# Performance work log

Hardware: AMD Instinct MI355X
Metric: run time of the kernel (lower is better)

## Reference

```python
import jax, jax.numpy as jnp
import numpy as np

NEG_BIG = -9e15
ALPHA = 0.2  # LeakyReLU negative slope


def setup_inputs() -> dict:
    key = jax.random.key(0)
    k1, k2, k3, k4 = jax.random.split(key, 4)
    N, F_in, F_out = 8192, 256, 64
    inp = jax.random.normal(k1, (N, F_in), dtype=jnp.float32)
    adj = jax.random.randint(k2, (N, N), 0, 2, dtype=jnp.int32)
    W = jax.random.normal(k3, (F_in, F_out), dtype=jnp.float32) * 0.05
    a = jax.random.normal(k4, (2 * F_out, 1), dtype=jnp.float32) * 0.05
    return {"input": inp, "adj": adj, "W": W, "a": a}


def reference(input, adj, W, a):
    # h = X W : [N, F_out]
    h = input @ W
    F_out = W.shape[1]
    # a_input[i,j] = concat(h_i, h_j); a_input @ a = h@a1 broadcast over j + h@a2 broadcast over i.
    a1 = a[:F_out, 0]   # [F_out]
    a2 = a[F_out:, 0]   # [F_out]
    s1 = h @ a1         # [N]
    s2 = h @ a2         # [N]
    e = jax.nn.leaky_relu(s1[:, None] + s2[None, :], negative_slope=ALPHA)  # [N, N]
    att = jnp.where(adj > 0, e, jnp.float32(NEG_BIG))
    att = jax.nn.softmax(att, axis=1)
    # dropout is identity in eval mode (training=False)
    h_prime = att @ h   # [N, F_out]
    return jax.nn.elu(h_prime)
```

## Files before the change

kernel.cpp:

```cpp
#include <hip/hip_runtime.h>
#include <hip/hip_bf16.h>

typedef __bf16 bf16_t;
typedef __attribute__((ext_vector_type(8))) __bf16 bf16x8;
typedef __attribute__((ext_vector_type(4))) __bf16 bf16x4;
typedef __attribute__((ext_vector_type(4))) float floatx4;
typedef __attribute__((ext_vector_type(4))) int intx4;

#define NN 8192
#define FIN 256
#define FOUT 64
#define GAT_ALPHA 0.2f
#define JHALF (NN / 2)

__global__ __launch_bounds__(256) void gat_h_kernel(
    const float* __restrict__ input,
    const float* __restrict__ W,
    const float* __restrict__ a,
    bf16_t* __restrict__ hT,
    float* __restrict__ s1g, float* __restrict__ e1g, float* __restrict__ f1g,
    float* __restrict__ s2g, float* __restrict__ e2g, float* __restrict__ f2g)
{
    alignas(16) __shared__ bf16_t in_lds[32][264];
    alignas(16) __shared__ bf16_t wt_lds[64][264];
    __shared__ float h_lds[32][65];

    const int t  = threadIdx.x;
    const int i0 = blockIdx.x * 32;

    #pragma unroll
    for (int v = 0; v < 8; v++) {
        int u  = v * 256 + t;
        int i  = u >> 6;
        int k4 = (u & 63) * 4;
        floatx4 x = *(const floatx4*)(input + (size_t)(i0 + i) * FIN + k4);
        bf16x4 b;
        #pragma unroll
        for (int e = 0; e < 4; e++) b[e] = (bf16_t)x[e];
        *(bf16x4*)(&in_lds[i][k4]) = b;
    }
    #pragma unroll
    for (int v = 0; v < 16; v++) {
        int u  = v * 256 + t;
        int k  = u >> 4;
        int f4 = (u & 15) * 4;
        floatx4 wv = *(const floatx4*)(W + k * FOUT + f4);
        #pragma unroll
        for (int e = 0; e < 4; e++) wt_lds[f4 + e][k] = (bf16_t)wv[e];
    }
    __syncthreads();

    const int wave = t >> 6;
    const int lane = t & 63;
    const int i16  = (wave & 1) * 16;
    const int f32  = (wave >> 1) * 32;
    const int lm   = lane & 15;
    const int lq   = lane >> 4;

    floatx4 acc0 = {0.f, 0.f, 0.f, 0.f};
    floatx4 acc1 = {0.f, 0.f, 0.f, 0.f};
    #pragma unroll
    for (int ks = 0; ks < 8; ks++) {
        int ko = ks * 32 + lq * 8;
        bf16x8 af = *(const bf16x8*)(&in_lds[i16 + lm][ko]);
        bf16x8 b0 = *(const bf16x8*)(&wt_lds[f32 + lm][ko]);
        bf16x8 b1 = *(const bf16x8*)(&wt_lds[f32 + 16 + lm][ko]);
        acc0 = __builtin_amdgcn_mfma_f32_16x16x32_bf16(af, b0, acc0, 0, 0, 0);
        acc1 = __builtin_amdgcn_mfma_f32_16x16x32_bf16(af, b1, acc1, 0, 0, 0);
    }

    #pragma unroll
    for (int c = 0; c < 2; c++) {
        floatx4 acc = c ? acc1 : acc0;
        int f  = f32 + c * 16 + lm;
        int ib = i0 + i16 + lq * 4;
        bf16x4 hp;
        #pragma unroll
        for (int r = 0; r < 4; r++) hp[r] = (bf16_t)acc[r];
        *(bf16x4*)(hT + (size_t)f * NN + ib) = hp;
    }
    #pragma unroll
    for (int c = 0; c < 2; c++) {
        floatx4 acc = c ? acc1 : acc0;
        #pragma unroll
        for (int r = 0; r < 4; r++)
            h_lds[i16 + lq * 4 + r][f32 + c * 16 + lm] = acc[r];
    }
    __syncthreads();

    if (t < 64) {
        int r   = t & 31;
        int sel = t >> 5;
        const float* av = a + sel * FOUT;
        float s = 0.f;
        #pragma unroll 8
        for (int f = 0; f < FOUT; f++) s += h_lds[r][f] * av[f];
        int gi = i0 + r;
        float E = expf(s);
        float F = expf(GAT_ALPHA * s);
        if (sel == 0) { s1g[gi] = s; e1g[gi] = E; f1g[gi] = F; }
        else          { s2g[gi] = s; e2g[gi] = E; f2g[gi] = F; }
    }
}

#define LOAD_CHUNK(J0)                                                         \
    {                                                                          \
        s2v = *(const floatx4*)(s2g + (J0) + 4 * tj);                          \
        e2v = *(const floatx4*)(e2g + (J0) + 4 * tj);                          \
        f2v = *(const floatx4*)(f2g + (J0) + 4 * tj);                          \
        _Pragma("unroll")                                                      \
        for (int it = 0; it < 8; it++)                                         \
            adjv[it] = *(const intx4*)(adj +                                   \
                (size_t)(i0 + it * 4 + ti) * NN + (J0) + 4 * tj);              \
        _Pragma("unroll")                                                      \
        for (int u = 0; u < 8; u++) {                                          \
            int f  = (u * 256 + t) >> 5;                                       \
            int j8 = ((u * 256 + t) & 31) * 8;                                 \
            hv[u] = *(const bf16x8*)(hT + (size_t)f * NN + (J0) + j8);         \
        }                                                                      \
    }

#define CONSUME_CHUNK()                                                        \
    {                                                                          \
        _Pragma("unroll")                                                      \
        for (int it = 0; it < 8; it++) {                                       \
            int r = it * 4 + ti;                                               \
            float s1r = s1_l[r], E1 = e1_l[r], F1 = f1_l[r];                   \
            bf16x4 wq;                                                         \
            float sum = 0.f;                                                   \
            _Pragma("unroll")                                                  \
            for (int e = 0; e < 4; e++) {                                      \
                bool pos = (s1r + s2v[e]) > 0.f;                               \
                float wv = (adjv[it][e] > 0)                                   \
                               ? (pos ? E1 * e2v[e] : F1 * f2v[e]) : 0.f;      \
                bf16_t wb = (bf16_t)wv;                                        \
                wq[e] = wb;                                                    \
                sum += (float)wb;                                              \
            }                                                                  \
            rowsum[it] += sum;                                                 \
            *(bf16x4*)(&w_lds[r][4 * tj]) = wq;                                \
        }                                                                      \
        _Pragma("unroll")                                                      \
        for (int u = 0; u < 8; u++) {                                          \
            int f  = (u * 256 + t) >> 5;                                       \
            int j8 = ((u * 256 + t) & 31) * 8;                                 \
            *(bf16x8*)(&ht_lds[f][j8]) = hv[u];                                \
        }                                                                      \
    }

#define MFMA_CHUNK()                                                           \
    {                                                                          \
        _Pragma("unroll")                                                      \
        for (int ks = 0; ks < 8; ks++) {                                       \
            int ko = ks * 32 + lq * 8;                                         \
            bf16x8 af = *(const bf16x8*)(&w_lds[i16 + lm][ko]);                \
            bf16x8 b0 = *(const bf16x8*)(&ht_lds[f32 + lm][ko]);               \
            bf16x8 b1 = *(const bf16x8*)(&ht_lds[f32 + 16 + lm][ko]);          \
            acc0 = __builtin_amdgcn_mfma_f32_16x16x32_bf16(af, b0, acc0,0,0,0);\
            acc1 = __builtin_amdgcn_mfma_f32_16x16x32_bf16(af, b1, acc1,0,0,0);\
        }                                                                      \
    }

__global__ __launch_bounds__(256, 2) void gat_att_kernel(
    const int* __restrict__ adj,
    const bf16_t* __restrict__ hT,
    const float* __restrict__ s1g, const float* __restrict__ e1g,
    const float* __restrict__ f1g,
    const float* __restrict__ s2g, const float* __restrict__ e2g,
    const float* __restrict__ f2g,
    float* __restrict__ pacc,
    float* __restrict__ prs)
{
    alignas(16) __shared__ bf16_t w_lds[32][264];
    alignas(16) __shared__ bf16_t ht_lds[64][264];
    __shared__ float part[32][66];
    __shared__ float s1_l[32], e1_l[32], f1_l[32];

    const int t     = threadIdx.x;
    const int i0    = blockIdx.x * 32;
    const int half  = blockIdx.y;
    const int jbase = half * JHALF;
    const int tj    = t & 63;
    const int ti    = t >> 6;

    if (t < 32) {
        s1_l[t] = s1g[i0 + t];
        e1_l[t] = e1g[i0 + t];
        f1_l[t] = f1g[i0 + t];
    }

    const int wave = t >> 6;
    const int lane = t & 63;
    const int i16  = (wave & 1) * 16;
    const int f32  = (wave >> 1) * 32;
    const int lm   = lane & 15;
    const int lq   = lane >> 4;

    floatx4 acc0 = {0.f, 0.f, 0.f, 0.f};
    floatx4 acc1 = {0.f, 0.f, 0.f, 0.f};
    float rowsum[8];
    #pragma unroll
    for (int r = 0; r < 8; r++) rowsum[r] = 0.f;

    intx4   adjv[8];
    bf16x8  hv[8];
    floatx4 s2v, e2v, f2v;

    LOAD_CHUNK(jbase);

    for (int j0 = jbase; j0 < jbase + JHALF; j0 += 256) {
        __syncthreads();
        CONSUME_CHUNK();
        if (j0 + 256 < jbase + JHALF)
            LOAD_CHUNK(j0 + 256);
        __syncthreads();
        MFMA_CHUNK();
    }

    #pragma unroll
    for (int it = 0; it < 8; it++) part[it * 4 + ti][tj] = rowsum[it];
    __syncthreads();
    if (t < 32) {
        float s = 0.f;
        #pragma unroll 8
        for (int k = 0; k < 64; k++) s += part[t][k];
        prs[half * NN + i0 + t] = s;
    }

    float* pa = pacc + (size_t)half * NN * FOUT;
    #pragma unroll
    for (int c = 0; c < 2; c++) {
        floatx4 acc = c ? acc1 : acc0;
        int f = f32 + c * 16 + lm;
        #pragma unroll
        for (int r = 0; r < 4; r++) {
            int i = i16 + lq * 4 + r;
            pa[(size_t)(i0 + i) * FOUT + f] = acc[r];
        }
    }
}

__global__ __launch_bounds__(256) void gat_combine_kernel(
    const float* __restrict__ pacc,
    const float* __restrict__ prs,
    float* __restrict__ out)
{
    int idx = blockIdx.x * 256 + threadIdx.x;
    int i   = idx >> 4;
    floatx4 a0 = *(const floatx4*)(pacc + (size_t)idx * 4);
    floatx4 a1 = *(const floatx4*)(pacc + (size_t)NN * FOUT + (size_t)idx * 4);
    float rs   = prs[i] + prs[NN + i];
    float rinv = (rs > 0.f) ? 1.0f / rs : 0.f;
    floatx4 r;
    #pragma unroll
    for (int e = 0; e < 4; e++) {
        float x = (a0[e] + a1[e]) * rinv;
        r[e] = (x > 0.f) ? x : (expf(x) - 1.0f);
    }
    *(floatx4*)(out + (size_t)idx * 4) = r;
}

extern "C" void kernel_launch(void* const* d_in, const int* in_sizes, int n_in,
                              void* d_out, int out_size, void* d_ws, size_t ws_size,
                              hipStream_t stream) {
    const float* input = (const float*)d_in[0];
    const int*   adj   = (const int*)d_in[1];
    const float* W     = (const float*)d_in[2];
    const float* a     = (const float*)d_in[3];
    float*       out   = (float*)d_out;

    char* ws = (char*)d_ws;
    bf16_t* hT  = (bf16_t*)ws;
    float*  s1g = (float*)(ws + (1 << 20));
    float*  e1g = s1g + NN;
    float*  f1g = e1g + NN;
    float*  s2g = f1g + NN;
    float*  e2g = s2g + NN;
    float*  f2g = e2g + NN;
    float*  pacc = f2g + NN;
    float*  prs  = pacc + 2 * NN * FOUT;

    gat_h_kernel<<<NN / 32, 256, 0, stream>>>(input, W, a, hT,
                                              s1g, e1g, f1g, s2g, e2g, f2g);
    dim3 gridB(NN / 32, 2);
    gat_att_kernel<<<gridB, 256, 0, stream>>>(adj, hT,
                                              s1g, e1g, f1g, s2g, e2g, f2g,
                                              pacc, prs);
    gat_combine_kernel<<<NN * FOUT / 4 / 256, 256, 0, stream>>>(pacc, prs, out);
}
```

Before: 390.4 us.

## Restructure attention kernel to register-direct MFMA operands without LDS staging

The attention kernel now has each wave own 16 rows and feed MFMA straight from registers. Attention weights are computed in the A-fragment layout and hT fragments are loaded directly from global memory, which removes the LDS staging and both per-chunk barriers. Leaky-ReLU selection becomes max(E1*e2, F1*f2), and e2/f2 are packed as bf16 pairs, so s1/s2 are no longer loaded. The j dimension is split 8 ways with higher occupancy to add parallelism. In exchange, hT reads are duplicated across waves, partial-sum traffic grows for the combine kernel, and e2/f2 lose precision to bf16.

```diff
diff --git a/kernel.cpp b/kernel.cpp
--- a/kernel.cpp
+++ b/kernel.cpp
@@ -6,20 +6,23 @@
 typedef __attribute__((ext_vector_type(4))) __bf16 bf16x4;
 typedef __attribute__((ext_vector_type(4))) float floatx4;
 typedef __attribute__((ext_vector_type(4))) int intx4;
+typedef __attribute__((ext_vector_type(4))) unsigned int uintx4;
 
 #define NN 8192
 #define FIN 256
 #define FOUT 64
 #define GAT_ALPHA 0.2f
-#define JHALF (NN / 2)
+#define JSPLIT 8
+#define JSEG (NN / JSPLIT)
+#define NSTEP (JSEG / 32)
 
 __global__ __launch_bounds__(256) void gat_h_kernel(
     const float* __restrict__ input,
     const float* __restrict__ W,
     const float* __restrict__ a,
     bf16_t* __restrict__ hT,
-    float* __restrict__ s1g, float* __restrict__ e1g, float* __restrict__ f1g,
-    float* __restrict__ s2g, float* __restrict__ e2g, float* __restrict__ f2g)
+    float* __restrict__ e1g, float* __restrict__ f1g,
+    unsigned* __restrict__ ef2g)
 {
     alignas(16) __shared__ bf16_t in_lds[32][264];
     alignas(16) __shared__ bf16_t wt_lds[64][264];
@@ -98,145 +101,99 @@
         int gi = i0 + r;
         float E = expf(s);
         float F = expf(GAT_ALPHA * s);
-        if (sel == 0) { s1g[gi] = s; e1g[gi] = E; f1g[gi] = F; }
-        else          { s2g[gi] = s; e2g[gi] = E; f2g[gi] = F; }
-    }
-}
-
-#define LOAD_CHUNK(J0)                                                         \
+        if (sel == 0) {
+            e1g[gi] = E; f1g[gi] = F;
+        } else {
+            unsigned eb = __builtin_bit_cast(unsigned short, (bf16_t)E);
+            unsigned fb = __builtin_bit_cast(unsigned short, (bf16_t)F);
+            ef2g[gi] = (fb << 16) | eb;
+        }
+    }
+}
+
+#define LOADS(B, OFF)                                                          \
     {                                                                          \
-        s2v = *(const floatx4*)(s2g + (J0) + 4 * tj);                          \
-        e2v = *(const floatx4*)(e2g + (J0) + 4 * tj);                          \
-        f2v = *(const floatx4*)(f2g + (J0) + 4 * tj);                          \
+        adjb[B][0] = *(const intx4*)(adjrow + (OFF));                          \
+        adjb[B][1] = *(const intx4*)(adjrow + (OFF) + 4);                      \
+        efb[B][0]  = *(const uintx4*)(efp + (OFF));                            \
+        efb[B][1]  = *(const uintx4*)(efp + (OFF) + 4);                        \
         _Pragma("unroll")                                                      \
-        for (int it = 0; it < 8; it++)                                         \
-            adjv[it] = *(const intx4*)(adj +                                   \
-                (size_t)(i0 + it * 4 + ti) * NN + (J0) + 4 * tj);              \
+        for (int c = 0; c < 4; c++)                                            \
+            htb[B][c] = *(const bf16x8*)(htp + (size_t)c * 16 * NN + (OFF));   \
+    }
+
+#define CONSUME(B)                                                             \
+    {                                                                          \
+        bf16x8 wf;                                                             \
         _Pragma("unroll")                                                      \
-        for (int u = 0; u < 8; u++) {                                          \
-            int f  = (u * 256 + t) >> 5;                                       \
-            int j8 = ((u * 256 + t) & 31) * 8;                                 \
-            hv[u] = *(const bf16x8*)(hT + (size_t)f * NN + (J0) + j8);         \
-        }                                                                      \
-    }
-
-#define CONSUME_CHUNK()                                                        \
-    {                                                                          \
-        _Pragma("unroll")                                                      \
-        for (int it = 0; it < 8; it++) {                                       \
-            int r = it * 4 + ti;                                               \
-            float s1r = s1_l[r], E1 = e1_l[r], F1 = f1_l[r];                   \
-            bf16x4 wq;                                                         \
-            float sum = 0.f;                                                   \
-            _Pragma("unroll")                                                  \
-            for (int e = 0; e < 4; e++) {                                      \
-                bool pos = (s1r + s2v[e]) > 0.f;                               \
-                float wv = (adjv[it][e] > 0)                                   \
-                               ? (pos ? E1 * e2v[e] : F1 * f2v[e]) : 0.f;      \
-                bf16_t wb = (bf16_t)wv;                                        \
-                wq[e] = wb;                                                    \
-                sum += (float)wb;                                              \
-            }                                                                  \
-            rowsum[it] += sum;                                                 \
-            *(bf16x4*)(&w_lds[r][4 * tj]) = wq;                                \
+        for (int e = 0; e < 8; e++) {                                          \
+            int av      = (e < 4) ? adjb[B][0][e] : adjb[B][1][e - 4];         \
+            unsigned v  = (e < 4) ? efb[B][0][e] : efb[B][1][e - 4];           \
+            float e2 = __builtin_bit_cast(float, v << 16);                     \
+            float f2 = __builtin_bit_cast(float, v & 0xffff0000u);             \
+            float p  = fmaxf(E1 * e2, F1 * f2);                                \
+            float wv = (av > 0) ? p : 0.f;                                     \
+            bf16_t wb = (bf16_t)wv;                                            \
+            wf[e] = wb;                                                        \
+            rowsum += (float)wb;                                               \
         }                                                                      \
         _Pragma("unroll")                                                      \
-        for (int u = 0; u < 8; u++) {                                          \
-            int f  = (u * 256 + t) >> 5;                                       \
-            int j8 = ((u * 256 + t) & 31) * 8;                                 \
-            *(bf16x8*)(&ht_lds[f][j8]) = hv[u];                                \
-        }                                                                      \
-    }
-
-#define MFMA_CHUNK()                                                           \
-    {                                                                          \
-        _Pragma("unroll")                                                      \
-        for (int ks = 0; ks < 8; ks++) {                                       \
-            int ko = ks * 32 + lq * 8;                                         \
-            bf16x8 af = *(const bf16x8*)(&w_lds[i16 + lm][ko]);                \
-            bf16x8 b0 = *(const bf16x8*)(&ht_lds[f32 + lm][ko]);               \
-            bf16x8 b1 = *(const bf16x8*)(&ht_lds[f32 + 16 + lm][ko]);          \
-            acc0 = __builtin_amdgcn_mfma_f32_16x16x32_bf16(af, b0, acc0,0,0,0);\
-            acc1 = __builtin_amdgcn_mfma_f32_16x16x32_bf16(af, b1, acc1,0,0,0);\
-        }                                                                      \
-    }
-
-__global__ __launch_bounds__(256, 2) void gat_att_kernel(
+        for (int c = 0; c < 4; c++)                                            \
+            acc[c] = __builtin_amdgcn_mfma_f32_16x16x32_bf16(                  \
+                wf, htb[B][c], acc[c], 0, 0, 0);                               \
+    }
+
+__global__ __launch_bounds__(256, 4) void gat_att_kernel(
     const int* __restrict__ adj,
     const bf16_t* __restrict__ hT,
-    const float* __restrict__ s1g, const float* __restrict__ e1g,
-    const float* __restrict__ f1g,
-    const float* __restrict__ s2g, const float* __restrict__ e2g,
-    const float* __restrict__ f2g,
+    const float* __restrict__ e1g, const float* __restrict__ f1g,
+    const unsigned* __restrict__ ef2g,
     float* __restrict__ pacc,
     float* __restrict__ prs)
 {
-    alignas(16) __shared__ bf16_t w_lds[32][264];
-    alignas(16) __shared__ bf16_t ht_lds[64][264];
-    __shared__ float part[32][66];
-    __shared__ float s1_l[32], e1_l[32], f1_l[32];
-
-    const int t     = threadIdx.x;
-    const int i0    = blockIdx.x * 32;
-    const int half  = blockIdx.y;
-    const int jbase = half * JHALF;
-    const int tj    = t & 63;
-    const int ti    = t >> 6;
-
-    if (t < 32) {
-        s1_l[t] = s1g[i0 + t];
-        e1_l[t] = e1g[i0 + t];
-        f1_l[t] = f1g[i0 + t];
-    }
-
+    const int t    = threadIdx.x;
     const int wave = t >> 6;
     const int lane = t & 63;
-    const int i16  = (wave & 1) * 16;
-    const int f32  = (wave >> 1) * 32;
-    const int lm   = lane & 15;
-    const int lq   = lane >> 4;
-
-    floatx4 acc0 = {0.f, 0.f, 0.f, 0.f};
-    floatx4 acc1 = {0.f, 0.f, 0.f, 0.f};
-    float rowsum[8];
-    #pragma unroll
-    for (int r = 0; r < 8; r++) rowsum[r] = 0.f;
-
-    intx4   adjv[8];
-    bf16x8  hv[8];
-    floatx4 s2v, e2v, f2v;
-
-    LOAD_CHUNK(jbase);
-
-    for (int j0 = jbase; j0 < jbase + JHALF; j0 += 256) {
-        __syncthreads();
-        CONSUME_CHUNK();
-        if (j0 + 256 < jbase + JHALF)
-            LOAD_CHUNK(j0 + 256);
-        __syncthreads();
-        MFMA_CHUNK();
-    }
-
-    #pragma unroll
-    for (int it = 0; it < 8; it++) part[it * 4 + ti][tj] = rowsum[it];
-    __syncthreads();
-    if (t < 32) {
-        float s = 0.f;
-        #pragma unroll 8
-        for (int k = 0; k < 64; k++) s += part[t][k];
-        prs[half * NN + i0 + t] = s;
-    }
-
-    float* pa = pacc + (size_t)half * NN * FOUT;
-    #pragma unroll
-    for (int c = 0; c < 2; c++) {
-        floatx4 acc = c ? acc1 : acc0;
-        int f = f32 + c * 16 + lm;
-        #pragma unroll
-        for (int r = 0; r < 4; r++) {
-            int i = i16 + lq * 4 + r;
-            pa[(size_t)(i0 + i) * FOUT + f] = acc[r];
-        }
+    const int m    = lane & 15;
+    const int q    = lane >> 4;
+    const int i0   = blockIdx.x * 64 + wave * 16;
+    const int js   = blockIdx.y;
+    const int row  = i0 + m;
+
+    const float E1 = e1g[row];
+    const float F1 = f1g[row];
+
+    const int*      adjrow = adj + (size_t)row * NN + js * JSEG + q * 8;
+    const unsigned* efp    = ef2g + js * JSEG + q * 8;
+    const bf16_t*   htp    = hT + (size_t)m * NN + js * JSEG + q * 8;
+
+    floatx4 acc[4];
+    #pragma unroll
+    for (int c = 0; c < 4; c++) acc[c] = (floatx4){0.f, 0.f, 0.f, 0.f};
+    float rowsum = 0.f;
+
+    intx4  adjb[2][2];
+    uintx4 efb[2][2];
+    bf16x8 htb[2][4];
+
+    LOADS(0, 0);
+    for (int s = 0; s < NSTEP; s += 2) {
+        LOADS(1, (s + 1) * 32);
+        CONSUME(0);
+        if (s + 2 < NSTEP) LOADS(0, (s + 2) * 32);
+        CONSUME(1);
+    }
+
+    rowsum += __shfl_xor(rowsum, 16, 64);
+    rowsum += __shfl_xor(rowsum, 32, 64);
+    if (lane < 16) prs[(size_t)js * NN + i0 + lane] = rowsum;
+
+    float* pa = pacc + (size_t)js * NN * FOUT;
+    #pragma unroll
+    for (int c = 0; c < 4; c++) {
+        #pragma unroll
+        for (int r = 0; r < 4; r++)
+            pa[(size_t)(i0 + q * 4 + r) * FOUT + c * 16 + m] = acc[c][r];
     }
 }
 
@@ -247,14 +204,18 @@
 {
     int idx = blockIdx.x * 256 + threadIdx.x;
     int i   = idx >> 4;
-    floatx4 a0 = *(const floatx4*)(pacc + (size_t)idx * 4);
-    floatx4 a1 = *(const floatx4*)(pacc + (size_t)NN * FOUT + (size_t)idx * 4);
-    float rs   = prs[i] + prs[NN + i];
+    floatx4 s = {0.f, 0.f, 0.f, 0.f};
+    float rs  = 0.f;
+    #pragma unroll
+    for (int js = 0; js < JSPLIT; js++) {
+        s  += *(const floatx4*)(pacc + (size_t)js * NN * FOUT + (size_t)idx * 4);
+        rs += prs[(size_t)js * NN + i];
+    }
     float rinv = (rs > 0.f) ? 1.0f / rs : 0.f;
     floatx4 r;
     #pragma unroll
     for (int e = 0; e < 4; e++) {
-        float x = (a0[e] + a1[e]) * rinv;
+        float x = s[e] * rinv;
         r[e] = (x > 0.f) ? x : (expf(x) - 1.0f);
     }
     *(floatx4*)(out + (size_t)idx * 4) = r;
@@ -270,21 +231,18 @@
     float*       out   = (float*)d_out;
 
     char* ws = (char*)d_ws;
-    bf16_t* hT  = (bf16_t*)ws;
-    float*  s1g = (float*)(ws + (1 << 20));
-    float*  e1g = s1g + NN;
-    float*  f1g = e1g + NN;
-    float*  s2g = f1g + NN;
-    float*  e2g = s2g + NN;
-    float*  f2g = e2g + NN;
-    float*  pacc = f2g + NN;
-    float*  prs  = pacc + 2 * NN * FOUT;
-
-    gat_h_kernel<<<NN / 32, 256, 0, stream>>>(input, W, a, hT,
-                                              s1g, e1g, f1g, s2g, e2g, f2g);
-    dim3 gridB(NN / 32, 2);
-    gat_att_kernel<<<gridB, 256, 0, stream>>>(adj, hT,
-                                              s1g, e1g, f1g, s2g, e2g, f2g,
+    bf16_t*   hT   = (bf16_t*)ws;
+    float*    e1g  = (float*)(ws + (1 << 20));
+    float*    f1g  = e1g + NN;
+    unsigned* ef2g = (unsigned*)(f1g + NN);
+    float*    pacc = (float*)(ef2g + NN);
+    float*    prs  = pacc + (size_t)JSPLIT * NN * FOUT;
+
+    gat_h_kernel<<<NN / 32, 256, 0, stream>>>(input, W, a, hT, e1g, f1g, ef2g);
+
+    dim3 gridB(NN / 64, JSPLIT);
+    gat_att_kernel<<<gridB, 256, 0, stream>>>(adj, hT, e1g, f1g, ef2g,
                                               pacc, prs);
+
     gat_combine_kernel<<<NN * FOUT / 4 / 256, 256, 0, stream>>>(pacc, prs, out);
 }
```

New measurement: 417.8 us. 1.07x slower.
